# Kernel optimization log

Measured on AMD Instinct MI355X. Metric: run time of the kernel, lower is better.

## Reference

```python
import jax, jax.numpy as jnp
from jax import lax
import numpy as np


def _box_sum(x, k):
    # zero-padded sliding-window sum over last two dims of [B, H, W];
    # 'SAME' padding with additive identity 0 exactly matches nn.Unfold's
    # zero padding of k//2 on each side for odd k.
    return lax.reduce_window(x, 0.0, lax.add, (1, k, k), (1, 1, 1), 'SAME')


def _local_std(x, k):
    # torch.std over the k*k patch dim is the unbiased (n-1) sample std;
    # fused one-pass form: var = (sum(x^2) - sum(x)^2/n) / (n-1)
    n = float(k * k)
    s1 = _box_sum(x, k)
    s2 = _box_sum(x * x, k)
    var = (s2 - s1 * s1 / n) / (n - 1.0)
    return jnp.sqrt(jnp.maximum(var, 0.0))


def setup_inputs() -> dict:
    key = jax.random.key(0)
    k1, k2 = jax.random.split(key)
    B, C, H, W = 8, 6, 1024, 1024
    predictions = jax.random.normal(k1, (B, C, H, W), dtype=jnp.float32)
    targets = jax.random.randint(k2, (B, H, W), 0, C, dtype=jnp.int64)
    return {"predictions": predictions, "targets": targets, "kernel_size": 5}


def reference(predictions, targets, kernel_size):
    k = int(kernel_size)
    pred_classes = jnp.argmax(predictions, axis=1).astype(jnp.float32)  # [B,H,W]
    tgt = targets.astype(jnp.float32)                                    # [B,H,W]
    pred_consistency = _local_std(pred_classes, k)
    target_consistency = _local_std(tgt, k)
    return jnp.mean((pred_consistency - target_consistency) ** 2)
```

## Files before the change

### kernel.cpp

```cpp
#include <hip/hip_runtime.h>

#define IMG_H 1024
#define IMG_W 1024
#define HW    (IMG_H * IMG_W)
#define HW4   (HW / 4)
#define NCLS  6
#define NBATCH 8
#define TH 8
#define HR 12
#define CSW 1032

typedef float fv4 __attribute__((ext_vector_type(4)));
typedef int   iv4 __attribute__((ext_vector_type(4)));

__device__ __forceinline__ fv4 ntload_f4(const float* p) {
  return __builtin_nontemporal_load((const fv4*)p);
}
__device__ __forceinline__ iv4 ntload_i4(const int* p) {
  return __builtin_nontemporal_load((const iv4*)p);
}

__global__ __launch_bounds__(256) void argmax_pack_kernel(
    const float* __restrict__ pred, const int* __restrict__ tgt,
    unsigned char* __restrict__ packed) {
  const int gtid = blockIdx.x * 256 + threadIdx.x;
  const int wave = gtid >> 6;
  const int lane = gtid & 63;
  const int img  = wave >> 10;
  const int G0   = (wave & 1023) * 256;
  const float* pb = pred + (size_t)img * NCLS * HW;
  const int*   tb = tgt  + (size_t)img * HW;

  int g[4];
#pragma unroll
  for (int j = 0; j < 4; ++j) g[j] = G0 + j * 64 + lane;

  fv4 best[4];
  iv4 idx[4];
#pragma unroll
  for (int j = 0; j < 4; ++j) {
    best[j] = ntload_f4(pb + (size_t)g[j] * 4);
    idx[j] = (iv4)0;
  }
#pragma unroll
  for (int c = 1; c < NCLS; ++c) {
    fv4 v[4];
#pragma unroll
    for (int j = 0; j < 4; ++j)
      v[j] = ntload_f4(pb + ((size_t)c * HW4 + g[j]) * 4);
#pragma unroll
    for (int j = 0; j < 4; ++j) {
#pragma unroll
      for (int e = 0; e < 4; ++e) {
        if (v[j][e] > best[j][e]) { best[j][e] = v[j][e]; idx[j][e] = c; }
      }
    }
  }
  iv4 t[4];
#pragma unroll
  for (int j = 0; j < 4; ++j) t[j] = ntload_i4(tb + (size_t)g[j] * 4);
#pragma unroll
  for (int j = 0; j < 4; ++j) {
    uchar4 o;
    o.x = (unsigned char)(idx[j][0] | (t[j][0] << 3));
    o.y = (unsigned char)(idx[j][1] | (t[j][1] << 3));
    o.z = (unsigned char)(idx[j][2] | (t[j][2] << 3));
    o.w = (unsigned char)(idx[j][3] | (t[j][3] << 3));
    ((uchar4*)packed)[(size_t)img * HW4 + g[j]] = o;
  }
}

__global__ __launch_bounds__(256, 4) void stencil_loss_kernel(
    const unsigned int* __restrict__ packed32, float* __restrict__ out) {
  __shared__ unsigned int halo32[HR * 256];
  __shared__ unsigned int colsum[4 * CSW];
  __shared__ float wsum[4];

  const int tid = threadIdx.x;
  const int job = blockIdx.x;
  const int img = job >> 7;
  const int y0  = (job & 127) * TH;
  const unsigned int* pw = packed32 + (size_t)img * (HW / 4);

  if (tid < 32) {
    const int r = tid >> 3, j = tid & 7;
    colsum[r * CSW + ((j < 4) ? j : 1024 + j)] = 0u;
  }

  for (int k = 0; k < HR * 256; k += 256) {
    const int id  = k + tid;
    const int row = id >> 8;
    const int g   = id & 255;
    const int gy  = y0 + row - 2;
    unsigned int w = 0u;
    if ((unsigned)gy < IMG_H) w = pw[gy * 256 + g];
    halo32[row * 256 + g] = w;
  }
  __syncthreads();

  float acc = 0.f;
#pragma unroll
  for (int bb = 0; bb < 2; ++bb) {
    for (int k = 0; k < 4 * 256; k += 256) {
      const int id = k + tid;
      const int r  = id >> 8;
      const int g  = id & 255;
      const unsigned int* h = &halo32[(bb * 4 + r) * 256 + g];
      unsigned s1p[4] = {0,0,0,0}, s2p[4] = {0,0,0,0};
      unsigned s1t[4] = {0,0,0,0}, s2t[4] = {0,0,0,0};
#pragma unroll
      for (int d = 0; d < 5; ++d) {
        const unsigned wv = h[d * 256];
#pragma unroll
        for (int j = 0; j < 4; ++j) {
          const unsigned pv = (wv >> (8 * j)) & 7u;
          const unsigned tv = (wv >> (8 * j + 3)) & 7u;
          s1p[j] += pv; s2p[j] += pv * pv;
          s1t[j] += tv; s2t[j] += tv * tv;
        }
      }
      uint4 o;
      o.x = s1p[0] | (s2p[0] << 8) | (s1t[0] << 16) | (s2t[0] << 24);
      o.y = s1p[1] | (s2p[1] << 8) | (s1t[1] << 16) | (s2t[1] << 24);
      o.z = s1p[2] | (s2p[2] << 8) | (s1t[2] << 16) | (s2t[2] << 24);
      o.w = s1p[3] | (s2p[3] << 8) | (s1t[3] << 16) | (s2t[3] << 24);
      *(uint4*)&colsum[r * CSW + 4 + 4 * g] = o;
    }
    __syncthreads();

    for (int k = 0; k < 4 * 256; k += 256) {
      const int id = k + tid;
      const int r  = id >> 8;
      const int g  = id & 255;
      const unsigned int* cs = &colsum[r * CSW + 4 * g];
      const uint4 wa = *(const uint4*)(cs);
      const uint4 wb = *(const uint4*)(cs + 4);
      const uint4 wc = *(const uint4*)(cs + 8);
      const unsigned w[12] = {wa.x, wa.y, wa.z, wa.w,
                              wb.x, wb.y, wb.z, wb.w,
                              wc.x, wc.y, wc.z, wc.w};
#pragma unroll
      for (int j = 0; j < 4; ++j) {
        int s1p = 0, s2p = 0, s1t = 0, s2t = 0;
#pragma unroll
        for (int d = 0; d < 5; ++d) {
          const unsigned v = w[j + 2 + d];
          s1p += (int)(v & 0xFFu);
          s2p += (int)((v >> 8) & 0xFFu);
          s1t += (int)((v >> 16) & 0xFFu);
          s2t += (int)(v >> 24);
        }
        const float varp = (float)(25 * s2p - s1p * s1p) * (1.0f / 600.0f);
        const float vart = (float)(25 * s2t - s1t * s1t) * (1.0f / 600.0f);
        const float dd = sqrtf(varp) - sqrtf(vart);
        acc += dd * dd;
      }
    }
    __syncthreads();
  }

#pragma unroll
  for (int off = 32; off > 0; off >>= 1) acc += __shfl_down(acc, off, 64);
  const int lane = tid & 63;
  const int wid  = tid >> 6;
  if (lane == 0) wsum[wid] = acc;
  __syncthreads();
  if (tid == 0) {
    const float t = wsum[0] + wsum[1] + wsum[2] + wsum[3];
    atomicAdd(out, t * (1.0f / 8388608.0f));
  }
}

extern "C" void kernel_launch(void* const* d_in, const int* in_sizes, int n_in,
                              void* d_out, int out_size, void* d_ws, size_t ws_size,
                              hipStream_t stream) {
  const float* pred = (const float*)d_in[0];
  const int* tgt    = (const int*)d_in[1];
  float* out = (float*)d_out;
  unsigned char* packed = (unsigned char*)d_ws;

  (void)hipMemsetAsync(d_out, 0, sizeof(float), stream);

  argmax_pack_kernel<<<dim3(2048), dim3(256), 0, stream>>>(pred, tgt, packed);

  stencil_loss_kernel<<<dim3(1024), dim3(256), 0, stream>>>(
      (const unsigned int*)packed, out);
}
```

Measured before the change: 303.1 us.

## Use SWAR byte-packed sums and perm-based squares in stencil kernel

Rewrites the vertical and horizontal box-sum passes to handle four packed pixels per 32-bit word in SIMD-within-a-register style. Squares come from a byte permute lookup table, and horizontal sliding sums use alignbyte shifts. The column-sum buffer is split into separate shared arrays for s1 and s2 of prediction and target, with s2 widened to 16-bit lanes so the 5-row sums of squares cannot overflow. This cuts per-pixel ALU work and shared-memory traffic, at the cost of more intricate packing logic and somewhat more LDS usage.

New measurement: 299.9 us. Within noise of the previous version (-1.1%).

```diff
diff --git a/kernel.cpp b/kernel.cpp
--- a/kernel.cpp
+++ b/kernel.cpp
@@ -8,7 +8,8 @@
 #define NBATCH 8
 #define TH 8
 #define HR 12
-#define CSW 1032
+#define CS1W 260
+#define CS2W 516
 
 typedef float fv4 __attribute__((ext_vector_type(4)));
 typedef int   iv4 __attribute__((ext_vector_type(4)));
@@ -73,7 +74,10 @@
 __global__ __launch_bounds__(256, 4) void stencil_loss_kernel(
     const unsigned int* __restrict__ packed32, float* __restrict__ out) {
   __shared__ unsigned int halo32[HR * 256];
-  __shared__ unsigned int colsum[4 * CSW];
+  __shared__ unsigned int cs1p[4 * CS1W];
+  __shared__ unsigned int cs1t[4 * CS1W];
+  __shared__ unsigned int cs2p[4 * CS2W];
+  __shared__ unsigned int cs2t[4 * CS2W];
   __shared__ float wsum[4];
 
   const int tid = threadIdx.x;
@@ -82,9 +86,12 @@
   const int y0  = (job & 127) * TH;
   const unsigned int* pw = packed32 + (size_t)img * (HW / 4);
 
-  if (tid < 32) {
-    const int r = tid >> 3, j = tid & 7;
-    colsum[r * CSW + ((j < 4) ? j : 1024 + j)] = 0u;
+  {
+    const int r = tid >> 6, L = tid & 63;
+    if (L < 2)       cs1p[r * CS1W + (L ? 257 : 0)] = 0u;
+    else if (L < 4)  cs1t[r * CS1W + ((L - 2) ? 257 : 0)] = 0u;
+    else if (L < 8)  { const int m = L - 4; cs2p[r * CS2W + (m < 2 ? m : 512 + m)] = 0u; }
+    else if (L < 12) { const int m = L - 8; cs2t[r * CS2W + (m < 2 ? m : 512 + m)] = 0u; }
   }
 
   for (int k = 0; k < HR * 256; k += 256) {
@@ -98,60 +105,91 @@
   }
   __syncthreads();
 
+  const unsigned M7  = 0x07070707u;
+  const unsigned MFF = 0x00FF00FFu;
+  const unsigned SQHI = 0x00001910u;
+  const unsigned SQLO = 0x09040100u;
+
   float acc = 0.f;
 #pragma unroll
   for (int bb = 0; bb < 2; ++bb) {
-    for (int k = 0; k < 4 * 256; k += 256) {
-      const int id = k + tid;
-      const int r  = id >> 8;
-      const int g  = id & 255;
-      const unsigned int* h = &halo32[(bb * 4 + r) * 256 + g];
-      unsigned s1p[4] = {0,0,0,0}, s2p[4] = {0,0,0,0};
-      unsigned s1t[4] = {0,0,0,0}, s2t[4] = {0,0,0,0};
+#pragma unroll
+    for (int r = 0; r < 4; ++r) {
+      const unsigned int* h = &halo32[(bb * 4 + r) * 256 + tid];
+      unsigned s1p = 0u, s1t = 0u, s2p = 0u, s2t = 0u;
 #pragma unroll
       for (int d = 0; d < 5; ++d) {
-        const unsigned wv = h[d * 256];
-#pragma unroll
-        for (int j = 0; j < 4; ++j) {
-          const unsigned pv = (wv >> (8 * j)) & 7u;
-          const unsigned tv = (wv >> (8 * j + 3)) & 7u;
-          s1p[j] += pv; s2p[j] += pv * pv;
-          s1t[j] += tv; s2t[j] += tv * tv;
-        }
-      }
-      uint4 o;
-      o.x = s1p[0] | (s2p[0] << 8) | (s1t[0] << 16) | (s2t[0] << 24);
-      o.y = s1p[1] | (s2p[1] << 8) | (s1t[1] << 16) | (s2t[1] << 24);
-      o.z = s1p[2] | (s2p[2] << 8) | (s1t[2] << 16) | (s2t[2] << 24);
-      o.w = s1p[3] | (s2p[3] << 8) | (s1t[3] << 16) | (s2t[3] << 24);
-      *(uint4*)&colsum[r * CSW + 4 + 4 * g] = o;
+        const unsigned w  = h[d * 256];
+        const unsigned wp = w & M7;
+        const unsigned wt = (w >> 3) & M7;
+        s1p += wp; s1t += wt;
+        s2p += __builtin_amdgcn_perm(SQHI, SQLO, wp);
+        s2t += __builtin_amdgcn_perm(SQHI, SQLO, wt);
+      }
+      cs1p[r * CS1W + tid + 1] = s1p;
+      cs1t[r * CS1W + tid + 1] = s1t;
+      {
+        const unsigned pl = s2p & MFF, ph = (s2p >> 8) & MFF;
+        uint2 o;
+        o.x = (pl & 0xFFFFu) | (ph << 16);
+        o.y = (pl >> 16) | (ph & 0xFFFF0000u);
+        *(uint2*)&cs2p[r * CS2W + 2 + 2 * tid] = o;
+      }
+      {
+        const unsigned tl = s2t & MFF, th = (s2t >> 8) & MFF;
+        uint2 o;
+        o.x = (tl & 0xFFFFu) | (th << 16);
+        o.y = (tl >> 16) | (th & 0xFFFF0000u);
+        *(uint2*)&cs2t[r * CS2W + 2 + 2 * tid] = o;
+      }
     }
     __syncthreads();
 
-    for (int k = 0; k < 4 * 256; k += 256) {
-      const int id = k + tid;
-      const int r  = id >> 8;
-      const int g  = id & 255;
-      const unsigned int* cs = &colsum[r * CSW + 4 * g];
-      const uint4 wa = *(const uint4*)(cs);
-      const uint4 wb = *(const uint4*)(cs + 4);
-      const uint4 wc = *(const uint4*)(cs + 8);
-      const unsigned w[12] = {wa.x, wa.y, wa.z, wa.w,
-                              wb.x, wb.y, wb.z, wb.w,
-                              wc.x, wc.y, wc.z, wc.w};
+#pragma unroll
+    for (int r = 0; r < 4; ++r) {
+      const unsigned* ap = &cs1p[r * CS1W + tid];
+      const unsigned pw0 = ap[0], pw1 = ap[1], pw2 = ap[2];
+      const unsigned Vp = __builtin_amdgcn_alignbyte(pw1, pw0, 2)
+                        + __builtin_amdgcn_alignbyte(pw1, pw0, 3)
+                        + pw1
+                        + __builtin_amdgcn_alignbyte(pw2, pw1, 1)
+                        + __builtin_amdgcn_alignbyte(pw2, pw1, 2);
+      const unsigned* at = &cs1t[r * CS1W + tid];
+      const unsigned tw0 = at[0], tw1 = at[1], tw2 = at[2];
+      const unsigned Vt = __builtin_amdgcn_alignbyte(tw1, tw0, 2)
+                        + __builtin_amdgcn_alignbyte(tw1, tw0, 3)
+                        + tw1
+                        + __builtin_amdgcn_alignbyte(tw2, tw1, 1)
+                        + __builtin_amdgcn_alignbyte(tw2, tw1, 2);
+
+      const uint2* bp = (const uint2*)&cs2p[r * CS2W + 2 * tid];
+      const uint2 pe0 = bp[0], pe1 = bp[1], pe2 = bp[2];
+      const unsigned pd0 = pe0.y, pd1 = pe1.x, pd2 = pe1.y, pd3 = pe2.x;
+      const unsigned pP1 = __builtin_amdgcn_alignbyte(pd1, pd0, 2);
+      const unsigned pP3 = __builtin_amdgcn_alignbyte(pd2, pd1, 2);
+      const unsigned pQ3 = __builtin_amdgcn_alignbyte(pd3, pd2, 2);
+      const unsigned pA = pd0 + pP1 + pd1 + pP3 + pd2;
+      const unsigned pB = pd1 + pP3 + pd2 + pQ3 + pd3;
+
+      const uint2* bt = (const uint2*)&cs2t[r * CS2W + 2 * tid];
+      const uint2 te0 = bt[0], te1 = bt[1], te2 = bt[2];
+      const unsigned td0 = te0.y, td1 = te1.x, td2 = te1.y, td3 = te2.x;
+      const unsigned tP1 = __builtin_amdgcn_alignbyte(td1, td0, 2);
+      const unsigned tP3 = __builtin_amdgcn_alignbyte(td2, td1, 2);
+      const unsigned tQ3 = __builtin_amdgcn_alignbyte(td3, td2, 2);
+      const unsigned tA = td0 + tP1 + td1 + tP3 + td2;
+      const unsigned tB = td1 + tP3 + td2 + tQ3 + td3;
+
 #pragma unroll
       for (int j = 0; j < 4; ++j) {
-        int s1p = 0, s2p = 0, s1t = 0, s2t = 0;
-#pragma unroll
-        for (int d = 0; d < 5; ++d) {
-          const unsigned v = w[j + 2 + d];
-          s1p += (int)(v & 0xFFu);
-          s2p += (int)((v >> 8) & 0xFFu);
-          s1t += (int)((v >> 16) & 0xFFu);
-          s2t += (int)(v >> 24);
-        }
-        const float varp = (float)(25 * s2p - s1p * s1p) * (1.0f / 600.0f);
-        const float vart = (float)(25 * s2t - s1t * s1t) * (1.0f / 600.0f);
+        const int s1pj = (int)((Vp >> (8 * j)) & 0xFFu);
+        const int s1tj = (int)((Vt >> (8 * j)) & 0xFFu);
+        const int s2pj = (int)(j == 0 ? (pA & 0xFFFFu) : j == 1 ? (pA >> 16)
+                             : j == 2 ? (pB & 0xFFFFu) : (pB >> 16));
+        const int s2tj = (int)(j == 0 ? (tA & 0xFFFFu) : j == 1 ? (tA >> 16)
+                             : j == 2 ? (tB & 0xFFFFu) : (tB >> 16));
+        const float varp = (float)(25 * s2pj - s1pj * s1pj) * (1.0f / 600.0f);
+        const float vart = (float)(25 * s2tj - s1tj * s1tj) * (1.0f / 600.0f);
         const float dd = sqrtf(varp) - sqrtf(vart);
         acc += dd * dd;
       }
```
